# Kernel tuning notes

Measured on AMD Instinct MI355X. Metric: run time of the kernel, lower is better.

Reference implementation:

```python
import jax, jax.numpy as jnp
import numpy as np

B, S, D, H = 2, 2048, 1024, 16
DK = D // H


def setup_inputs() -> dict:
    key = jax.random.key(0)
    ks = jax.random.split(key, 12)
    scale = 1.0 / np.sqrt(D)
    inp = {
        "query": jax.random.normal(ks[0], (B, S, D), jnp.float32),
        "key_in": jax.random.normal(ks[1], (B, S, D), jnp.float32),
        "value": jax.random.normal(ks[2], (B, S, D), jnp.float32),
        "mask": jnp.ones((1, 1, S, S), dtype=bool),
        "w_q": jax.random.normal(ks[3], (D, D), jnp.float32) * scale,
        "b_q": jnp.zeros((D,), jnp.float32),
        "w_k": jax.random.normal(ks[4], (D, D), jnp.float32) * scale,
        "b_k": jnp.zeros((D,), jnp.float32),
        "w_v": jax.random.normal(ks[5], (D, D), jnp.float32) * scale,
        "b_v": jnp.zeros((D,), jnp.float32),
        "w_o": jax.random.normal(ks[6], (D, D), jnp.float32) * scale,
        "b_o": jnp.zeros((D,), jnp.float32),
    }
    return inp


def reference(query, key_in, value, mask, w_q, b_q, w_k, b_k, w_v, b_v, w_o, b_o):
    # QKV projections (nn.Linear: x @ W.T + b; here weights stored as [D_in, D_out])
    q = query @ w_q + b_q          # [B, S, D]
    k = key_in @ w_k + b_k
    v = value @ w_v + b_v
    # split heads -> [B, H, S, DK]
    q = q.reshape(B, S, H, DK).transpose(0, 2, 1, 3)
    k = k.reshape(B, S, H, DK).transpose(0, 2, 1, 3)
    v = v.reshape(B, S, H, DK).transpose(0, 2, 1, 3)
    # scaled dot-product attention (naive: full [B,H,S,S] scores)
    scores = jnp.einsum('bhqd,bhkd->bhqk', q, k) / jnp.sqrt(jnp.float32(DK))
    scores = jnp.where(mask, scores, jnp.float32(-1e9))
    probs = jax.nn.softmax(scores, axis=-1)  # dropout p=0.0 -> identity
    x = jnp.einsum('bhqk,bhkd->bhqd', probs, v)  # [B, H, S, DK]
    x = x.transpose(0, 2, 1, 3).reshape(B, S, D)
    return x @ w_o + b_o
```

## Files before the change

kernel.cpp:

```cpp
#include <hip/hip_runtime.h>
#include <cstdint>
#include <cstddef>


typedef _Float16 f16_t;
typedef _Float16 f16x8 __attribute__((ext_vector_type(8)));
typedef _Float16 f16x4 __attribute__((ext_vector_type(4)));
typedef float    f32x4 __attribute__((ext_vector_type(4)));
typedef unsigned int u32x2 __attribute__((ext_vector_type(2)));

#define S_LEN 2048
#define DMODEL 1024
#define NHEAD 16
#define DK 64
#define NKV (S_LEN / 64)

__device__ __forceinline__ void async_copy16(void* lds, const void* g) {
    __builtin_amdgcn_global_load_lds(
        (const __attribute__((address_space(1))) unsigned int*)g,
        (__attribute__((address_space(3))) unsigned int*)lds,
        16, 0, 0);
}

__device__ __forceinline__ float fexp2(float x) {
#if __has_builtin(__builtin_amdgcn_exp2f)
    return __builtin_amdgcn_exp2f(x);
#else
    return exp2f(x);
#endif
}

__device__ __forceinline__ unsigned int cvt_pk_u32(float a, float b) {
#if __has_builtin(__builtin_amdgcn_cvt_pkrtz)
    return __builtin_bit_cast(unsigned int, __builtin_amdgcn_cvt_pkrtz(a, b));
#else
    union { f16_t h[2]; unsigned int u; } r;
    r.h[0] = (f16_t)a; r.h[1] = (f16_t)b; return r.u;
#endif
}

__global__ __launch_bounds__(256) void cvt3_kernel(
    const float* __restrict__ s0, const float* __restrict__ s1, const float* __restrict__ s2,
    f16_t* __restrict__ d0, f16_t* __restrict__ d1, f16_t* __restrict__ d2, int n)
{
    const float* s = blockIdx.y == 0 ? s0 : blockIdx.y == 1 ? s1 : s2;
    f16_t*       d = blockIdx.y == 0 ? d0 : blockIdx.y == 1 ? d1 : d2;
    int i = (blockIdx.x * 256 + threadIdx.x) * 4;
    if (i + 3 < n) {
        f32x4 v = *(const f32x4*)(s + i);
        f16x4 o;
        o[0] = (f16_t)v[0]; o[1] = (f16_t)v[1];
        o[2] = (f16_t)v[2]; o[3] = (f16_t)v[3];
        *(f16x4*)(d + i) = o;
    }
}

__global__ __launch_bounds__(256) void transpose_cvt_kernel(
    const float* __restrict__ w0, const float* __restrict__ w1,
    const float* __restrict__ w2, const float* __restrict__ w3,
    f16_t* __restrict__ wt_base)
{
    __shared__ float tile[32][33];
    int z = blockIdx.z;
    const float* w = z == 0 ? w0 : z == 1 ? w1 : z == 2 ? w2 : w3;
    f16_t* wt = wt_base + (size_t)z * DMODEL * DMODEL;
    int tx = threadIdx.x, ty = threadIdx.y;
    int bx = blockIdx.x * 32;
    int by = blockIdx.y * 32;
#pragma unroll
    for (int i = 0; i < 4; ++i)
        tile[ty + i * 8][tx] = w[(size_t)(bx + ty + i * 8) * DMODEL + by + tx];
    __syncthreads();
#pragma unroll
    for (int i = 0; i < 4; ++i)
        wt[(size_t)(by + ty + i * 8) * DMODEL + bx + tx] = (f16_t)tile[tx][ty + i * 8];
}

__global__ __launch_bounds__(256) void qkv_gemm_kernel(
    const f16_t* __restrict__ Aq, const f16_t* __restrict__ Ak, const f16_t* __restrict__ Av,
    const f16_t* __restrict__ Bt,
    const float* __restrict__ bq, const float* __restrict__ bk, const float* __restrict__ bv,
    f16_t* __restrict__ q_h, f16_t* __restrict__ k_h, f16_t* __restrict__ v_t)
{
    __shared__ f16_t As[128 * 32];
    __shared__ f16_t Bs[128 * 32];

    int tid  = threadIdx.x;
    int lane = tid & 63;
    int w    = tid >> 6;
    int wm   = w >> 1, wn = w & 1;

    int lin = blockIdx.y * 24 + blockIdx.x;
    int swz = (lin & 7) * 96 + (lin >> 3);
    int bx  = swz % 24, by = swz / 24;
    int row0 = by * 128;
    int col0 = bx * 128;
    int which = col0 >> 10;
    const f16_t* A = which == 0 ? Aq : which == 1 ? Ak : Av;
    const float* bias = which == 0 ? bq : which == 1 ? bk : bv;

    f32x4 acc[4][4] = {};

    for (int kk = 0; kk < 1024; kk += 32) {
        __syncthreads();
#pragma unroll
        for (int j = 0; j < 2; ++j) {
            int c = w * 2 + j;
            int r = c * 16 + (lane >> 2);
            int e = (lane & 3) * 8;
            async_copy16(&As[c * 512], A  + (size_t)(row0 + r) * 1024 + kk + e);
            async_copy16(&Bs[c * 512], Bt + (size_t)(col0 + r) * 1024 + kk + e);
        }
        __syncthreads();

        f16x8 a[4], b[4];
#pragma unroll
        for (int mi = 0; mi < 4; ++mi)
            a[mi] = *(const f16x8*)&As[(wm * 64 + mi * 16 + (lane & 15)) * 32 + (lane >> 4) * 8];
#pragma unroll
        for (int ni = 0; ni < 4; ++ni)
            b[ni] = *(const f16x8*)&Bs[(wn * 64 + ni * 16 + (lane & 15)) * 32 + (lane >> 4) * 8];
#pragma unroll
        for (int mi = 0; mi < 4; ++mi)
#pragma unroll
            for (int ni = 0; ni < 4; ++ni)
                acc[mi][ni] = __builtin_amdgcn_mfma_f32_16x16x32_f16(a[mi], b[ni], acc[mi][ni], 0, 0, 0);
    }

    const float QSCALE = 0.125f * 1.4426950408889634f;
    if (which == 2) {
#pragma unroll
        for (int mi = 0; mi < 4; ++mi) {
#pragma unroll
            for (int ni = 0; ni < 4; ++ni) {
                int ss0  = row0 + wm * 64 + mi * 16 + (lane >> 4) * 4;
                int gcol = col0 + wn * 64 + ni * 16 + (lane & 15);
                int nc   = gcol & 1023;
                float bv4 = bv[nc];
                int bb = ss0 >> 11, ss = ss0 & 2047;
                int hh = nc >> 6,   dd = nc & 63;
                f16x4 vv;
#pragma unroll
                for (int r = 0; r < 4; ++r)
                    vv[r] = (f16_t)(acc[mi][ni][r] + bv4);
                *(f16x4*)&v_t[((size_t)(bb * NHEAD + hh) * DK + dd) * S_LEN + ss] = vv;
            }
        }
    } else {
#pragma unroll
        for (int mi = 0; mi < 4; ++mi) {
#pragma unroll
            for (int ni = 0; ni < 4; ++ni) {
#pragma unroll
                for (int r = 0; r < 4; ++r) {
                    int grow = row0 + wm * 64 + mi * 16 + (lane >> 4) * 4 + r;
                    int gcol = col0 + wn * 64 + ni * 16 + (lane & 15);
                    int nc   = gcol & 1023;
                    float v  = acc[mi][ni][r] + bias[nc];
                    int bb = grow >> 11, ss = grow & 2047;
                    int hh = nc >> 6,    dd = nc & 63;
                    if (which == 0)
                        q_h[(((size_t)(bb * NHEAD + hh) * S_LEN + ss) << 6) + dd] = (f16_t)(v * QSCALE);
                    else
                        k_h[(((size_t)(bb * NHEAD + hh) * S_LEN + ss) << 6) + dd] = (f16_t)v;
                }
            }
        }
    }
}

__global__ __launch_bounds__(256) void out_gemm_kernel(
    const f16_t* __restrict__ A, const f16_t* __restrict__ Bt,
    const float* __restrict__ bias, float* __restrict__ outp)
{
    __shared__ f16_t As[64 * 32];
    __shared__ f16_t Bs[128 * 32];

    int tid  = threadIdx.x;
    int lane = tid & 63;
    int w    = tid >> 6;
    int wm   = w >> 1, wn = w & 1;

    int lin = blockIdx.y * 8 + blockIdx.x;
    int swz = (lin & 7) * 64 + (lin >> 3);
    int row0 = (swz >> 3) * 64;
    int col0 = (swz & 7) * 128;

    f32x4 acc[2][4] = {};

    for (int kk = 0; kk < 1024; kk += 32) {
        __syncthreads();
        {
            int r = (lane >> 2);
            int e = (lane & 3) * 8;
            async_copy16(&As[w * 512], A + (size_t)(row0 + w * 16 + r) * 1024 + kk + e);
#pragma unroll
            for (int j = 0; j < 2; ++j) {
                int c = w * 2 + j;
                async_copy16(&Bs[c * 512], Bt + (size_t)(col0 + c * 16 + r) * 1024 + kk + e);
            }
        }
        __syncthreads();

        f16x8 a[2], b[4];
#pragma unroll
        for (int mi = 0; mi < 2; ++mi)
            a[mi] = *(const f16x8*)&As[(wm * 32 + mi * 16 + (lane & 15)) * 32 + (lane >> 4) * 8];
#pragma unroll
        for (int ni = 0; ni < 4; ++ni)
            b[ni] = *(const f16x8*)&Bs[(wn * 64 + ni * 16 + (lane & 15)) * 32 + (lane >> 4) * 8];
#pragma unroll
        for (int mi = 0; mi < 2; ++mi)
#pragma unroll
            for (int ni = 0; ni < 4; ++ni)
                acc[mi][ni] = __builtin_amdgcn_mfma_f32_16x16x32_f16(a[mi], b[ni], acc[mi][ni], 0, 0, 0);
    }

#pragma unroll
    for (int mi = 0; mi < 2; ++mi)
#pragma unroll
        for (int ni = 0; ni < 4; ++ni)
#pragma unroll
            for (int r = 0; r < 4; ++r) {
                int grow = row0 + wm * 32 + mi * 16 + (lane >> 4) * 4 + r;
                int gcol = col0 + wn * 64 + ni * 16 + (lane & 15);
                outp[(size_t)grow * 1024 + gcol] = acc[mi][ni][r] + bias[gcol];
            }
}

__global__ __launch_bounds__(256) void flash_kernel(
    const f16_t* __restrict__ Q, const f16_t* __restrict__ K,
    const f16_t* __restrict__ Vt, f16_t* __restrict__ Ao)
{
    __shared__ f16_t Kl[2][64 * 64];
    __shared__ f16_t Vl[64 * 64];
    __shared__ f16_t Pw[4][16 * 72];

    int tid  = threadIdx.x;
    int lane = tid & 63;
    int li   = lane & 15;
    int g    = lane >> 4;
    int w    = tid >> 6;

    int lin = blockIdx.y * 32 + blockIdx.x;
    int swz = (lin & 7) * 128 + (lin >> 3);
    int qt  = swz & 31;
    int bh  = swz >> 5;

    const size_t hbase = (size_t)bh * S_LEN * DK;
    const f16_t* Qh = Q  + hbase;
    const f16_t* Kh = K  + hbase;
    const f16_t* Vh = Vt + hbase;

    int q0 = qt * 64 + w * 16;

    f16x8 aq[2];
#pragma unroll
    for (int kc = 0; kc < 2; ++kc)
        aq[kc] = *(const f16x8*)(Qh + (size_t)(q0 + li) * DK + kc * 32 + g * 8);

    f16x8 ones;
#pragma unroll
    for (int i = 0; i < 8; ++i) ones[i] = (f16_t)1.0f;

    f32x4 ot[4] = {};
    f32x4 lacc = {};
    float mrun = -1e30f;

    int lr  = lane >> 3;
    int sl8 = ((lane & 7) ^ lr) * 8;
    const f16_t* srcK = Kh + (size_t)(w * 16 + lr) * 64    + sl8;
    const f16_t* srcV = Vh + (size_t)(w * 16 + lr) * S_LEN + sl8;

    auto stageV = [&](int kt) {
        async_copy16(&Vl[(w * 16) * 64],     srcV + kt * 64);
        async_copy16(&Vl[(w * 16 + 8) * 64], srcV + 8 * S_LEN + kt * 64);
    };
    auto stageK = [&](int buf, int kt) {
        const f16_t* p = srcK + (size_t)kt * 4096;
        async_copy16(&Kl[buf][(w * 16) * 64],     p);
        async_copy16(&Kl[buf][(w * 16 + 8) * 64], p + 512);
    };

    int x0 = li * 64 + ((g    ) ^ (li & 7)) * 8;
    int x1 = li * 64 + ((4 + g) ^ (li & 7)) * 8;
    int pww = li * 72 + g * 4;
    int pwr = li * 72 + g * 8;

    stageK(0, 0);
    int cur = 0;

    for (int kt = 0; kt < NKV; ++kt) {
        __syncthreads();
        stageV(kt);
        if (kt + 1 < NKV) stageK(cur ^ 1, kt + 1);

        f32x4 s[4] = {};
        __builtin_amdgcn_s_setprio(1);
#pragma unroll
        for (int kc = 0; kc < 2; ++kc)
#pragma unroll
            for (int kn = 0; kn < 4; ++kn) {
                f16x8 ak = *(const f16x8*)&Kl[cur][kn * 1024 + (kc ? x1 : x0)];
                s[kn] = __builtin_amdgcn_mfma_f32_16x16x32_f16(ak, aq[kc], s[kn], 0, 0, 0);
            }
        __builtin_amdgcn_s_setprio(0);

        {
            float mx = fmaxf(s[0][0], s[0][1]);
            mx = fmaxf(fmaxf(mx, s[0][2]), s[0][3]);
            mx = fmaxf(fmaxf(mx, s[1][0]), s[1][1]);
            mx = fmaxf(fmaxf(mx, s[1][2]), s[1][3]);
            mx = fmaxf(fmaxf(mx, s[2][0]), s[2][1]);
            mx = fmaxf(fmaxf(mx, s[2][2]), s[2][3]);
            mx = fmaxf(fmaxf(mx, s[3][0]), s[3][1]);
            mx = fmaxf(fmaxf(mx, s[3][2]), s[3][3]);
            mx = fmaxf(mx, __shfl_xor(mx, 16));
            mx = fmaxf(mx, __shfl_xor(mx, 32));
            if (!__all(mx - mrun <= 8.0f)) {
                float mn = fmaxf(mrun, mx);
                float alpha = fexp2(mrun - mn);
                mrun = mn;
#pragma unroll
                for (int r = 0; r < 4; ++r) lacc[r] *= alpha;
#pragma unroll
                for (int nd = 0; nd < 4; ++nd)
#pragma unroll
                    for (int r = 0; r < 4; ++r)
                        ot[nd][r] *= alpha;
            }
#pragma unroll
            for (int kn = 0; kn < 4; ++kn) {
                u32x2 pv;
                pv[0] = cvt_pk_u32(fexp2(s[kn][0] - mrun), fexp2(s[kn][1] - mrun));
                pv[1] = cvt_pk_u32(fexp2(s[kn][2] - mrun), fexp2(s[kn][3] - mrun));
                *(u32x2*)&Pw[w][pww + kn * 16] = pv;
            }
        }

        if (kt + 1 < NKV) asm volatile("s_waitcnt vmcnt(2)" ::: "memory");
        else              asm volatile("s_waitcnt vmcnt(0)" ::: "memory");

        __builtin_amdgcn_s_setprio(1);
#pragma unroll
        for (int kc = 0; kc < 2; ++kc) {
            f16x8 bp = *(const f16x8*)&Pw[w][pwr + kc * 32];
            lacc = __builtin_amdgcn_mfma_f32_16x16x32_f16(ones, bp, lacc, 0, 0, 0);
#pragma unroll
            for (int nd = 0; nd < 4; ++nd) {
                f16x8 av = *(const f16x8*)&Vl[nd * 1024 + (kc ? x1 : x0)];
                ot[nd] = __builtin_amdgcn_mfma_f32_16x16x32_f16(av, bp, ot[nd], 0, 0, 0);
            }
        }
        __builtin_amdgcn_s_setprio(0);

        cur ^= 1;
    }

    int b = bh >> 4, h = bh & 15;
    {
        float inv = 1.0f / lacc[0];
        int qrow = q0 + li;
        size_t base = (size_t)(b * S_LEN + qrow) * DMODEL + h * 64;
#pragma unroll
        for (int nd = 0; nd < 4; ++nd) {
            f16x4 ov;
#pragma unroll
            for (int r = 0; r < 4; ++r)
                ov[r] = (f16_t)(ot[nd][r] * inv);
            *(f16x4*)&Ao[base + nd * 16 + g * 4] = ov;
        }
    }
}

extern "C" void kernel_launch(void* const* d_in, const int* in_sizes, int n_in,
                              void* d_out, int out_size, void* d_ws, size_t ws_size,
                              hipStream_t stream)
{
    const float* query  = (const float*)d_in[0];
    const float* key_in = (const float*)d_in[1];
    const float* value  = (const float*)d_in[2];
    const float* w_q = (const float*)d_in[4];
    const float* b_q = (const float*)d_in[5];
    const float* w_k = (const float*)d_in[6];
    const float* b_k = (const float*)d_in[7];
    const float* w_v = (const float*)d_in[8];
    const float* b_v = (const float*)d_in[9];
    const float* w_o = (const float*)d_in[10];
    const float* b_o = (const float*)d_in[11];
    float* out = (float*)d_out;

    char* ws = (char*)d_ws;
    const size_t MB = 1024 * 1024;
    f16_t* x_q  = (f16_t*)(ws + 0 * MB);
    f16_t* x_k  = (f16_t*)(ws + 8 * MB);
    f16_t* x_v  = (f16_t*)(ws + 16 * MB);
    f16_t* wt   = (f16_t*)(ws + 24 * MB);
    f16_t* wt_o = (f16_t*)(ws + 30 * MB);
    f16_t* q_h  = (f16_t*)(ws + 32 * MB);
    f16_t* k_h  = (f16_t*)(ws + 40 * MB);
    f16_t* v_t  = (f16_t*)(ws + 48 * MB);
    f16_t* attn = (f16_t*)(ws + 56 * MB);

    const int n = 2 * S_LEN * DMODEL;

    cvt3_kernel<<<dim3(n / 1024, 3), 256, 0, stream>>>(query, key_in, value, x_q, x_k, x_v, n);
    transpose_cvt_kernel<<<dim3(32, 32, 4), dim3(32, 8), 0, stream>>>(w_q, w_k, w_v, w_o, wt);

    qkv_gemm_kernel<<<dim3(24, 32), 256, 0, stream>>>(
        x_q, x_k, x_v, wt, b_q, b_k, b_v, q_h, k_h, v_t);

    flash_kernel<<<dim3(32, 32), 256, 0, stream>>>(q_h, k_h, v_t, attn);

    out_gemm_kernel<<<dim3(8, 64), 256, 0, stream>>>(attn, wt_o, b_o, out);
}
```

Measured before the change: 151.6 us.

## Fuse fp32-to-fp16 input conversion into QKV GEMM and enlarge output GEMM tiles

```diff
diff --git a/kernel.cpp b/kernel.cpp
--- a/kernel.cpp
+++ b/kernel.cpp
@@ -37,22 +37,6 @@
     union { f16_t h[2]; unsigned int u; } r;
     r.h[0] = (f16_t)a; r.h[1] = (f16_t)b; return r.u;
 #endif
-}
-
-__global__ __launch_bounds__(256) void cvt3_kernel(
-    const float* __restrict__ s0, const float* __restrict__ s1, const float* __restrict__ s2,
-    f16_t* __restrict__ d0, f16_t* __restrict__ d1, f16_t* __restrict__ d2, int n)
-{
-    const float* s = blockIdx.y == 0 ? s0 : blockIdx.y == 1 ? s1 : s2;
-    f16_t*       d = blockIdx.y == 0 ? d0 : blockIdx.y == 1 ? d1 : d2;
-    int i = (blockIdx.x * 256 + threadIdx.x) * 4;
-    if (i + 3 < n) {
-        f32x4 v = *(const f32x4*)(s + i);
-        f16x4 o;
-        o[0] = (f16_t)v[0]; o[1] = (f16_t)v[1];
-        o[2] = (f16_t)v[2]; o[3] = (f16_t)v[3];
-        *(f16x4*)(d + i) = o;
-    }
 }
 
 __global__ __launch_bounds__(256) void transpose_cvt_kernel(
@@ -77,16 +61,18 @@
 }
 
 __global__ __launch_bounds__(256) void qkv_gemm_kernel(
-    const f16_t* __restrict__ Aq, const f16_t* __restrict__ Ak, const f16_t* __restrict__ Av,
+    const float* __restrict__ Aq, const float* __restrict__ Ak, const float* __restrict__ Av,
     const f16_t* __restrict__ Bt,
     const float* __restrict__ bq, const float* __restrict__ bk, const float* __restrict__ bv,
     f16_t* __restrict__ q_h, f16_t* __restrict__ k_h, f16_t* __restrict__ v_t)
 {
-    __shared__ f16_t As[128 * 32];
+    __shared__ float As[128 * 32];
     __shared__ f16_t Bs[128 * 32];
 
     int tid  = threadIdx.x;
     int lane = tid & 63;
+    int li   = lane & 15;
+    int g    = lane >> 4;
     int w    = tid >> 6;
     int wm   = w >> 1, wn = w & 1;
 
@@ -96,30 +82,47 @@
     int row0 = by * 128;
     int col0 = bx * 128;
     int which = col0 >> 10;
-    const f16_t* A = which == 0 ? Aq : which == 1 ? Ak : Av;
+    const float* A = which == 0 ? Aq : which == 1 ? Ak : Av;
     const float* bias = which == 0 ? bq : which == 1 ? bk : bv;
+
+    int lr  = lane >> 3;
+    int sl4 = ((lane & 7) ^ lr) * 4;
+    int rB  = lane >> 2;
+    int eB  = (lane & 3) * 8;
 
     f32x4 acc[4][4] = {};
 
     for (int kk = 0; kk < 1024; kk += 32) {
         __syncthreads();
 #pragma unroll
+        for (int j = 0; j < 4; ++j) {
+            int c = w * 4 + j;
+            int row = c * 8 + lr;
+            async_copy16(&As[c * 256], A + (size_t)(row0 + row) * 1024 + kk + sl4);
+        }
+#pragma unroll
         for (int j = 0; j < 2; ++j) {
             int c = w * 2 + j;
-            int r = c * 16 + (lane >> 2);
-            int e = (lane & 3) * 8;
-            async_copy16(&As[c * 512], A  + (size_t)(row0 + r) * 1024 + kk + e);
-            async_copy16(&Bs[c * 512], Bt + (size_t)(col0 + r) * 1024 + kk + e);
+            async_copy16(&Bs[c * 512], Bt + (size_t)(col0 + c * 16 + rB) * 1024 + kk + eB);
         }
         __syncthreads();
 
         f16x8 a[4], b[4];
 #pragma unroll
-        for (int mi = 0; mi < 4; ++mi)
-            a[mi] = *(const f16x8*)&As[(wm * 64 + mi * 16 + (lane & 15)) * 32 + (lane >> 4) * 8];
+        for (int mi = 0; mi < 4; ++mi) {
+            int row = wm * 64 + mi * 16 + li;
+            f32x4 lo = *(const f32x4*)&As[row * 32 + (((2 * g)     ^ (li & 7)) * 4)];
+            f32x4 hi = *(const f32x4*)&As[row * 32 + (((2 * g + 1) ^ (li & 7)) * 4)];
+            union { unsigned int u[4]; f16x8 v; } pk;
+            pk.u[0] = cvt_pk_u32(lo[0], lo[1]);
+            pk.u[1] = cvt_pk_u32(lo[2], lo[3]);
+            pk.u[2] = cvt_pk_u32(hi[0], hi[1]);
+            pk.u[3] = cvt_pk_u32(hi[2], hi[3]);
+            a[mi] = pk.v;
+        }
 #pragma unroll
         for (int ni = 0; ni < 4; ++ni)
-            b[ni] = *(const f16x8*)&Bs[(wn * 64 + ni * 16 + (lane & 15)) * 32 + (lane >> 4) * 8];
+            b[ni] = *(const f16x8*)&Bs[(wn * 64 + ni * 16 + li) * 32 + g * 8];
 #pragma unroll
         for (int mi = 0; mi < 4; ++mi)
 #pragma unroll
@@ -133,8 +136,8 @@
         for (int mi = 0; mi < 4; ++mi) {
 #pragma unroll
             for (int ni = 0; ni < 4; ++ni) {
-                int ss0  = row0 + wm * 64 + mi * 16 + (lane >> 4) * 4;
-                int gcol = col0 + wn * 64 + ni * 16 + (lane & 15);
+                int ss0  = row0 + wm * 64 + mi * 16 + g * 4;
+                int gcol = col0 + wn * 64 + ni * 16 + li;
                 int nc   = gcol & 1023;
                 float bv4 = bv[nc];
                 int bb = ss0 >> 11, ss = ss0 & 2047;
@@ -153,8 +156,8 @@
             for (int ni = 0; ni < 4; ++ni) {
 #pragma unroll
                 for (int r = 0; r < 4; ++r) {
-                    int grow = row0 + wm * 64 + mi * 16 + (lane >> 4) * 4 + r;
-                    int gcol = col0 + wn * 64 + ni * 16 + (lane & 15);
+                    int grow = row0 + wm * 64 + mi * 16 + g * 4 + r;
+                    int gcol = col0 + wn * 64 + ni * 16 + li;
                     int nc   = gcol & 1023;
                     float v  = acc[mi][ni][r] + bias[nc];
                     int bb = grow >> 11, ss = grow & 2047;
@@ -173,7 +176,7 @@
     const f16_t* __restrict__ A, const f16_t* __restrict__ Bt,
     const float* __restrict__ bias, float* __restrict__ outp)
 {
-    __shared__ f16_t As[64 * 32];
+    __shared__ f16_t As[128 * 32];
     __shared__ f16_t Bs[128 * 32];
 
     int tid  = threadIdx.x;
@@ -182,47 +185,45 @@
     int wm   = w >> 1, wn = w & 1;
 
     int lin = blockIdx.y * 8 + blockIdx.x;
-    int swz = (lin & 7) * 64 + (lin >> 3);
-    int row0 = (swz >> 3) * 64;
-    int col0 = (swz & 7) * 128;
-
-    f32x4 acc[2][4] = {};
+    int swz = (lin & 7) * 32 + (lin >> 3);
+    int row0 = (swz / 8) * 128;
+    int col0 = (swz % 8) * 128;
+
+    f32x4 acc[4][4] = {};
 
     for (int kk = 0; kk < 1024; kk += 32) {
         __syncthreads();
-        {
-            int r = (lane >> 2);
+#pragma unroll
+        for (int j = 0; j < 2; ++j) {
+            int c = w * 2 + j;
+            int r = c * 16 + (lane >> 2);
             int e = (lane & 3) * 8;
-            async_copy16(&As[w * 512], A + (size_t)(row0 + w * 16 + r) * 1024 + kk + e);
-#pragma unroll
-            for (int j = 0; j < 2; ++j) {
-                int c = w * 2 + j;
-                async_copy16(&Bs[c * 512], Bt + (size_t)(col0 + c * 16 + r) * 1024 + kk + e);
-            }
+            async_copy16(&As[c * 512], A  + (size_t)(row0 + r) * 1024 + kk + e);
+            async_copy16(&Bs[c * 512], Bt + (size_t)(col0 + r) * 1024 + kk + e);
         }
         __syncthreads();
 
-        f16x8 a[2], b[4];
-#pragma unroll
-        for (int mi = 0; mi < 2; ++mi)
-            a[mi] = *(const f16x8*)&As[(wm * 32 + mi * 16 + (lane & 15)) * 32 + (lane >> 4) * 8];
+        f16x8 a[4], b[4];
+#pragma unroll
+        for (int mi = 0; mi < 4; ++mi)
+            a[mi] = *(const f16x8*)&As[(wm * 64 + mi * 16 + (lane & 15)) * 32 + (lane >> 4) * 8];
 #pragma unroll
         for (int ni = 0; ni < 4; ++ni)
             b[ni] = *(const f16x8*)&Bs[(wn * 64 + ni * 16 + (lane & 15)) * 32 + (lane >> 4) * 8];
 #pragma unroll
-        for (int mi = 0; mi < 2; ++mi)
+        for (int mi = 0; mi < 4; ++mi)
 #pragma unroll
             for (int ni = 0; ni < 4; ++ni)
                 acc[mi][ni] = __builtin_amdgcn_mfma_f32_16x16x32_f16(a[mi], b[ni], acc[mi][ni], 0, 0, 0);
     }
 
 #pragma unroll
-    for (int mi = 0; mi < 2; ++mi)
+    for (int mi = 0; mi < 4; ++mi)
 #pragma unroll
         for (int ni = 0; ni < 4; ++ni)
 #pragma unroll
             for (int r = 0; r < 4; ++r) {
-                int grow = row0 + wm * 32 + mi * 16 + (lane >> 4) * 4 + r;
+                int grow = row0 + wm * 64 + mi * 16 + (lane >> 4) * 4 + r;
                 int gcol = col0 + wn * 64 + ni * 16 + (lane & 15);
                 outp[(size_t)grow * 1024 + gcol] = acc[mi][ni][r] + bias[gcol];
             }
@@ -392,9 +393,6 @@
 
     char* ws = (char*)d_ws;
     const size_t MB = 1024 * 1024;
-    f16_t* x_q  = (f16_t*)(ws + 0 * MB);
-    f16_t* x_k  = (f16_t*)(ws + 8 * MB);
-    f16_t* x_v  = (f16_t*)(ws + 16 * MB);
     f16_t* wt   = (f16_t*)(ws + 24 * MB);
     f16_t* wt_o = (f16_t*)(ws + 30 * MB);
     f16_t* q_h  = (f16_t*)(ws + 32 * MB);
@@ -402,15 +400,12 @@
     f16_t* v_t  = (f16_t*)(ws + 48 * MB);
     f16_t* attn = (f16_t*)(ws + 56 * MB);
 
-    const int n = 2 * S_LEN * DMODEL;
-
-    cvt3_kernel<<<dim3(n / 1024, 3), 256, 0, stream>>>(query, key_in, value, x_q, x_k, x_v, n);
     transpose_cvt_kernel<<<dim3(32, 32, 4), dim3(32, 8), 0, stream>>>(w_q, w_k, w_v, w_o, wt);
 
     qkv_gemm_kernel<<<dim3(24, 32), 256, 0, stream>>>(
-        x_q, x_k, x_v, wt, b_q, b_k, b_v, q_h, k_h, v_t);
+        query, key_in, value, wt, b_q, b_k, b_v, q_h, k_h, v_t);
 
     flash_kernel<<<dim3(32, 32), 256, 0, stream>>>(q_h, k_h, v_t, attn);
 
-    out_gemm_kernel<<<dim3(8, 64), 256, 0, stream>>>(attn, wt_o, b_o, out);
-}
+    out_gemm_kernel<<<dim3(8, 32), 256, 0, stream>>>(attn, wt_o, b_o, out);
+}
```

Measured after the change: 153.8 us. No clear change (+1.4%).
